# Optimization experiments

Hardware: AMD Instinct MI355X
Metric: run time of the kernel (lower is better)

## Reference

```python
import jax, jax.numpy as jnp
import numpy as np

B = 16; IMG = 127; INC = 64; GROUP = 1; STRIDE = 2; PAD = 1; KS = 3
G = INC // GROUP            # number of ScannCore blocks
S = KS * KS                 # patch_size (attention dim) = 9
SPN = (IMG + 2 * PAD - KS) // STRIDE + 1   # 64
PN = SPN * SPN              # patch_num = 4096
L = GROUP * PN              # sequence length per core


def setup_inputs() -> dict:
    key = jax.random.key(0)
    ks = jax.random.split(key, 9)
    sc = 1.0 / np.sqrt(S)
    x = jax.random.normal(ks[0], (B, INC, IMG, IMG), jnp.float32)
    Wq = jax.random.uniform(ks[1], (G, S, S), jnp.float32, -sc, sc)
    bq = jax.random.uniform(ks[2], (G, S), jnp.float32, -sc, sc)
    Wk = jax.random.uniform(ks[3], (G, S, S), jnp.float32, -sc, sc)
    bk = jax.random.uniform(ks[4], (G, S), jnp.float32, -sc, sc)
    Wv = jax.random.uniform(ks[5], (G, S, S), jnp.float32, -sc, sc)
    bv = jax.random.uniform(ks[6], (G, S), jnp.float32, -sc, sc)
    Wo = jax.random.uniform(ks[7], (G, S, 1), jnp.float32, -sc, sc)
    bo = jax.random.uniform(ks[8], (G, 1), jnp.float32, -sc, sc)
    return dict(x=x, Wq=Wq, bq=bq, Wk=Wk, bk=bk, Wv=Wv, bv=bv, Wo=Wo, bo=bo)


def reference(x, Wq, bq, Wk, bk, Wv, bv, Wo, bo):
    # F.unfold equivalent: [B, INC*S, SPN, SPN] with feature dim ordered (C, kh, kw)
    patches = jax.lax.conv_general_dilated_patches(
        x, (KS, KS), (STRIDE, STRIDE), [(PAD, PAD), (PAD, PAD)])
    t = patches.reshape(B, INC, S, PN)
    # split channels into G groups of GROUP, move patch axis before patch-pixel axis
    t = t.reshape(B, G, GROUP, S, PN).transpose(0, 1, 2, 4, 3).reshape(B, G, L, S)
    # batched tiny single-head attention across all G cores at once
    Q = jnp.einsum('bgls,gst->bglt', t, Wq) + bq[None, :, None, :]
    Km = jnp.einsum('bgls,gst->bglt', t, Wk) + bk[None, :, None, :]
    V = jnp.einsum('bgls,gst->bglt', t, Wv) + bv[None, :, None, :]
    # energy = K^T @ Q over the L axis -> [B, G, S, S]
    energy = jnp.einsum('bgls,bglt->bgst', Km, Q)
    attn = jax.nn.softmax(energy, axis=-1)   # dropout is identity in eval
    # (attn @ V^T)^T -> [B, G, L, S]
    a = jnp.einsum('bgst,bglt->bgls', attn, V)
    out = jnp.einsum('bgls,gso->bglo', a, Wo) + bo[None, :, None, :]  # [B,G,L,1]
    # faithful reshape/permute of original: [B, spn, spn, group] -> [B, group, spn, spn]
    out = out.reshape(B, G, SPN, SPN, GROUP).transpose(0, 1, 4, 2, 3)
    return out.reshape(B, INC, SPN, SPN)
```

## Files before the change

kernel.cpp:

```cpp
#include <hip/hip_runtime.h>
#include <math.h>

#define NB       16
#define IMG      127
#define PLANE    (IMG * IMG)
#define INC      64
#define PN       4096
#define NTHREADS 512
#define PPT      8

#define GLOBAL_AS __attribute__((address_space(1)))
#define LDS_AS    __attribute__((address_space(3)))

__device__ __forceinline__ constexpr int symidx(int p, int q) {
    return p * 9 - (p * (p - 1)) / 2 + (q - p);
}

__device__ __forceinline__ float wave_reduce_sum(float v) {
#define DPP_ADD(ctrl)                                                          \
    v += __builtin_bit_cast(float, __builtin_amdgcn_update_dpp(                \
             0, __builtin_bit_cast(int, v), (ctrl), 0xf, 0xf, true))
    DPP_ADD(0x111);
    DPP_ADD(0x112);
    DPP_ADD(0x114);
    DPP_ADD(0x118);
    DPP_ADD(0x142);
    DPP_ADD(0x143);
#undef DPP_ADD
    return v;
}

#define LOAD_ROW(d0, d1, d2, ihv)                                              \
    {                                                                          \
        const int  ih_ = (ihv);                                                \
        const bool rok = (unsigned)ih_ < (unsigned)IMG;                        \
        const int  ba  = ih_ * IMG + iw0;                                      \
        d0 = (rok && c0) ? plane[ba]     : 0.f;                                \
        d1 =  rok        ? plane[ba + 1] : 0.f;                                \
        d2 = (rok && c2) ? plane[ba + 2] : 0.f;                                \
    }

__global__ void __launch_bounds__(NTHREADS, 4)
scann_fused(const float* __restrict__ x,
            const float* __restrict__ Wq, const float* __restrict__ bq,
            const float* __restrict__ Wk, const float* __restrict__ bk,
            const float* __restrict__ Wv, const float* __restrict__ bv,
            const float* __restrict__ Wo, const float* __restrict__ bo,
            float* __restrict__ out)
{
    __shared__ float plane[PLANE];
    __shared__ float red[8 * 54];
    __shared__ float Msh[45];
    __shared__ float msh[9];
    __shared__ float MW[81];
    __shared__ float Wq_s[81], Wk_s[81], Wv_s[81];
    __shared__ float bq_s[9], bk_s[9], bv_s[9], Wo_s[9];
    __shared__ float en[81], at[81], wt[9], u_s[9];
    __shared__ float c_s, bo_sh;

    const int bg  = blockIdx.x;
    const int g   = bg & 63;
    const int tid = threadIdx.x;
    const int ow  = tid & 63;
    const int wv  = tid >> 6;
    const int oh0 = wv * PPT;

    const float* __restrict__ xp = x + (size_t)bg * PLANE;

    const int a0 = (4 - (bg & 3)) & 3;
    if (tid < a0) plane[tid] = xp[tid];
    #pragma unroll
    for (int j = 0; j < 7; ++j) {
        __builtin_amdgcn_global_load_lds(
            (const GLOBAL_AS void*)(xp + a0 + (j * NTHREADS + tid) * 4),
            (LDS_AS void*)(&plane[a0 + (j * NTHREADS + wv * 64) * 4]), 16, 0, 0);
    }
    {
        const int base = a0 + 7 * NTHREADS * 4;
        const int cnt  = PLANE - base;
        for (int i = tid; i < cnt; i += NTHREADS)
            plane[base + i] = xp[base + i];
    }

    if (tid < 81) {
        Wq_s[tid] = Wq[g * 81 + tid];
        Wk_s[tid] = Wk[g * 81 + tid];
        Wv_s[tid] = Wv[g * 81 + tid];
    } else if (tid >= 128 && tid < 137) {
        const int i = tid - 128;
        bq_s[i] = bq[g * 9 + i];
        bk_s[i] = bk[g * 9 + i];
        bv_s[i] = bv[g * 9 + i];
        Wo_s[i] = Wo[g * 9 + i];
    } else if (tid == 192) {
        bo_sh = bo[g];
    }
    __syncthreads();

    const int  iw0 = ow * 2 - 1;
    const bool c0  = (ow > 0), c2 = (ow < 63);
    const int  ih0 = oh0 * 2 - 1;

    {
        float mA[24], mm[9], v[9];
        #pragma unroll
        for (int i = 0; i < 24; ++i) mA[i] = 0.f;
        #pragma unroll
        for (int i = 0; i < 9; ++i)  mm[i] = 0.f;
        LOAD_ROW(v[0], v[1], v[2], ih0 + 0);
        LOAD_ROW(v[3], v[4], v[5], ih0 + 1);
        LOAD_ROW(v[6], v[7], v[8], ih0 + 2);
        #pragma unroll
        for (int k = 0; k < PPT; ++k) {
            #pragma unroll
            for (int p = 0; p < 9; ++p) mm[p] += v[p];
            int idx = 0;
            #pragma unroll
            for (int p = 0; p < 3; ++p)
                #pragma unroll
                for (int q = p; q < 9; ++q)
                    mA[idx++] += v[p] * v[q];
            if (k < PPT - 1) {
                v[0] = v[6]; v[1] = v[7]; v[2] = v[8];
                LOAD_ROW(v[3], v[4], v[5], ih0 + 2 * (k + 1) + 1);
                LOAD_ROW(v[6], v[7], v[8], ih0 + 2 * (k + 1) + 2);
            }
        }
        #pragma unroll
        for (int i = 0; i < 24; ++i) mA[i] = wave_reduce_sum(mA[i]);
        #pragma unroll
        for (int i = 0; i < 9; ++i)  mm[i] = wave_reduce_sum(mm[i]);
        if (ow == 63) {
            #pragma unroll
            for (int i = 0; i < 24; ++i) red[wv * 54 + i]      = mA[i];
            #pragma unroll
            for (int i = 0; i < 9; ++i)  red[wv * 54 + 45 + i] = mm[i];
        }
    }

    {
        float mB[21], v[9];
        #pragma unroll
        for (int i = 0; i < 21; ++i) mB[i] = 0.f;
        LOAD_ROW(v[0], v[1], v[2], ih0 + 0);
        LOAD_ROW(v[3], v[4], v[5], ih0 + 1);
        LOAD_ROW(v[6], v[7], v[8], ih0 + 2);
        #pragma unroll
        for (int k = 0; k < PPT; ++k) {
            int idx = 0;
            #pragma unroll
            for (int p = 3; p < 9; ++p)
                #pragma unroll
                for (int q = p; q < 9; ++q)
                    mB[idx++] += v[p] * v[q];
            if (k < PPT - 1) {
                v[0] = v[6]; v[1] = v[7]; v[2] = v[8];
                LOAD_ROW(v[3], v[4], v[5], ih0 + 2 * (k + 1) + 1);
                LOAD_ROW(v[6], v[7], v[8], ih0 + 2 * (k + 1) + 2);
            }
        }
        #pragma unroll
        for (int i = 0; i < 21; ++i) mB[i] = wave_reduce_sum(mB[i]);
        if (ow == 63) {
            #pragma unroll
            for (int i = 0; i < 21; ++i) red[wv * 54 + 24 + i] = mB[i];
        }
    }
    __syncthreads();

    if (wv == 0) {
        const int lane = ow;
        if (lane < 54) {
            float s = 0.f;
            #pragma unroll
            for (int w = 0; w < 8; ++w) s += red[w * 54 + lane];
            if (lane < 45) Msh[lane]      = s;
            else           msh[lane - 45] = s;
        }
        #pragma unroll
        for (int r = 0; r < 2; ++r) {
            const int e = lane + r * 64;
            if (e < 81) {
                const int p = e / 9, t = e % 9;
                float acc = 0.f;
                #pragma unroll
                for (int q = 0; q < 9; ++q) {
                    const int a_ = p < q ? p : q, b_ = p < q ? q : p;
                    acc += Msh[symidx(a_, b_)] * Wq_s[q * 9 + t];
                }
                MW[e] = acc;
            }
        }
        #pragma unroll
        for (int r = 0; r < 2; ++r) {
            const int e = lane + r * 64;
            if (e < 81) {
                const int s = e / 9, t = e % 9;
                float km = 0.f, qm = 0.f, acc = 0.f;
                #pragma unroll
                for (int p = 0; p < 9; ++p) {
                    km  += Wk_s[p * 9 + s] * msh[p];
                    qm  += Wq_s[p * 9 + t] * msh[p];
                    acc += Wk_s[p * 9 + s] * MW[p * 9 + t];
                }
                en[e] = acc + (float)PN * bk_s[s] * bq_s[t] + km * bq_s[t] + bk_s[s] * qm;
            }
        }
        if (lane < 9) {
            const int s = lane;
            float mx = en[s * 9];
            #pragma unroll
            for (int t = 1; t < 9; ++t) mx = fmaxf(mx, en[s * 9 + t]);
            float ex[9], sum = 0.f;
            #pragma unroll
            for (int t = 0; t < 9; ++t) { ex[t] = expf(en[s * 9 + t] - mx); sum += ex[t]; }
            const float inv = 1.f / sum;
            #pragma unroll
            for (int t = 0; t < 9; ++t) at[s * 9 + t] = ex[t] * inv;
        }
        if (lane < 9) {
            const int t = lane;
            float w = 0.f;
            #pragma unroll
            for (int s = 0; s < 9; ++s) w += at[s * 9 + t] * Wo_s[s];
            wt[t] = w;
        }
        if (lane < 9) {
            const int p = lane;
            float uu = 0.f;
            #pragma unroll
            for (int t = 0; t < 9; ++t) uu += Wv_s[p * 9 + t] * wt[t];
            u_s[p] = uu;
        }
        if (lane == 12) {
            float cc = bo_sh;
            #pragma unroll
            for (int t = 0; t < 9; ++t) cc += bv_s[t] * wt[t];
            c_s = cc;
        }
    }
    __syncthreads();

    float ur[9];
    #pragma unroll
    for (int i = 0; i < 9; ++i) ur[i] = u_s[i];
    const float cc = c_s;
    float* __restrict__ op = out + (size_t)bg * PN;

    {
        float v[9];
        LOAD_ROW(v[0], v[1], v[2], ih0 + 0);
        LOAD_ROW(v[3], v[4], v[5], ih0 + 1);
        LOAD_ROW(v[6], v[7], v[8], ih0 + 2);
        #pragma unroll
        for (int k = 0; k < PPT; ++k) {
            float o = cc;
            #pragma unroll
            for (int i = 0; i < 9; ++i) o += v[i] * ur[i];
            op[(oh0 + k) * 64 + ow] = o;
            if (k < PPT - 1) {
                v[0] = v[6]; v[1] = v[7]; v[2] = v[8];
                LOAD_ROW(v[3], v[4], v[5], ih0 + 2 * (k + 1) + 1);
                LOAD_ROW(v[6], v[7], v[8], ih0 + 2 * (k + 1) + 2);
            }
        }
    }
}

extern "C" void kernel_launch(void* const* d_in, const int* in_sizes, int n_in,
                              void* d_out, int out_size, void* d_ws, size_t ws_size,
                              hipStream_t stream) {
    (void)in_sizes; (void)n_in; (void)d_ws; (void)ws_size; (void)out_size;
    const float* x  = (const float*)d_in[0];
    const float* Wq = (const float*)d_in[1];
    const float* bq = (const float*)d_in[2];
    const float* Wk = (const float*)d_in[3];
    const float* bk = (const float*)d_in[4];
    const float* Wv = (const float*)d_in[5];
    const float* bv = (const float*)d_in[6];
    const float* Wo = (const float*)d_in[7];
    const float* bo = (const float*)d_in[8];
    float* out = (float*)d_out;

    dim3 grid(NB * INC), block(NTHREADS);
    hipLaunchKernelGGL(scann_fused, grid, block, 0, stream,
                       x, Wq, bq, Wk, bk, Wv, bv, Wo, bo, out);
}
```

Measured before the change: 41.09 us.

## Replace LDS plane staging with bounds-checked raw buffer loads from global

Drops the per-block copy of the whole input plane into shared memory. Each thread now reads its 3x3 patch rows straight from global memory through raw buffer loads, using the buffer's range check to return zero for out-of-bounds padding. Freeing that shared memory allows higher occupancy (launch bounds raised to 8) and cuts the wave reduction to 16-lane partial sums, with 32 slots combined through shared memory. The cost is that the input is read from global/L2 three times (two statistics passes and the output pass) rather than once, and each read depends on cache hit rates.

```diff
diff --git a/kernel.cpp b/kernel.cpp
--- a/kernel.cpp
+++ b/kernel.cpp
@@ -4,19 +4,23 @@
 #define NB       16
 #define IMG      127
 #define PLANE    (IMG * IMG)
+#define ROWB     (IMG * 4)
 #define INC      64
 #define PN       4096
 #define NTHREADS 512
 #define PPT      8
 
-#define GLOBAL_AS __attribute__((address_space(1)))
-#define LDS_AS    __attribute__((address_space(3)))
+typedef int int32x4 __attribute__((ext_vector_type(4)));
+
+__device__ float
+llvm_raw_buffer_load_f32(int32x4 srsrc, int voffset, int soffset, int aux)
+    __asm("llvm.amdgcn.raw.buffer.load.f32");
 
 __device__ __forceinline__ constexpr int symidx(int p, int q) {
     return p * 9 - (p * (p - 1)) / 2 + (q - p);
 }
 
-__device__ __forceinline__ float wave_reduce_sum(float v) {
+__device__ __forceinline__ float wave_reduce16(float v) {
 #define DPP_ADD(ctrl)                                                          \
     v += __builtin_bit_cast(float, __builtin_amdgcn_update_dpp(                \
              0, __builtin_bit_cast(int, v), (ctrl), 0xf, 0xf, true))
@@ -24,23 +28,22 @@
     DPP_ADD(0x112);
     DPP_ADD(0x114);
     DPP_ADD(0x118);
-    DPP_ADD(0x142);
-    DPP_ADD(0x143);
 #undef DPP_ADD
     return v;
 }
 
-#define LOAD_ROW(d0, d1, d2, ihv)                                              \
+#define LOAD_ROW_G(d0, d1, d2, vrow)                                           \
     {                                                                          \
-        const int  ih_ = (ihv);                                                \
-        const bool rok = (unsigned)ih_ < (unsigned)IMG;                        \
-        const int  ba  = ih_ * IMG + iw0;                                      \
-        d0 = (rok && c0) ? plane[ba]     : 0.f;                                \
-        d1 =  rok        ? plane[ba + 1] : 0.f;                                \
-        d2 = (rok && c2) ? plane[ba + 2] : 0.f;                                \
-    }
-
-__global__ void __launch_bounds__(NTHREADS, 4)
+        const int vr_ = (vrow);                                                \
+        const int r0_ = vr_ < 0 ? 0 : vr_;                                     \
+        d0 = llvm_raw_buffer_load_f32(srd, r0_,     0, 0);                     \
+        d1 = llvm_raw_buffer_load_f32(srd, vr_ + 4, 0, 0);                     \
+        d2 = llvm_raw_buffer_load_f32(srd, vr_ + 8, 0, 0);                     \
+        d0 = c0 ? d0 : 0.f;                                                    \
+        d2 = c2 ? d2 : 0.f;                                                    \
+    }
+
+__global__ void __launch_bounds__(NTHREADS, 8)
 scann_fused(const float* __restrict__ x,
             const float* __restrict__ Wq, const float* __restrict__ bq,
             const float* __restrict__ Wk, const float* __restrict__ bk,
@@ -48,8 +51,7 @@
             const float* __restrict__ Wo, const float* __restrict__ bo,
             float* __restrict__ out)
 {
-    __shared__ float plane[PLANE];
-    __shared__ float red[8 * 54];
+    __shared__ float red[32 * 54];
     __shared__ float Msh[45];
     __shared__ float msh[9];
     __shared__ float MW[81];
@@ -66,21 +68,8 @@
     const int oh0 = wv * PPT;
 
     const float* __restrict__ xp = x + (size_t)bg * PLANE;
-
-    const int a0 = (4 - (bg & 3)) & 3;
-    if (tid < a0) plane[tid] = xp[tid];
-    #pragma unroll
-    for (int j = 0; j < 7; ++j) {
-        __builtin_amdgcn_global_load_lds(
-            (const GLOBAL_AS void*)(xp + a0 + (j * NTHREADS + tid) * 4),
-            (LDS_AS void*)(&plane[a0 + (j * NTHREADS + wv * 64) * 4]), 16, 0, 0);
-    }
-    {
-        const int base = a0 + 7 * NTHREADS * 4;
-        const int cnt  = PLANE - base;
-        for (int i = tid; i < cnt; i += NTHREADS)
-            plane[base + i] = xp[base + i];
-    }
+    union { const float* p; unsigned int w[2]; } ba; ba.p = xp;
+    const int32x4 srd = { (int)ba.w[0], (int)ba.w[1], PLANE * 4, 0x00020000 };
 
     if (tid < 81) {
         Wq_s[tid] = Wq[g * 81 + tid];
@@ -95,11 +84,10 @@
     } else if (tid == 192) {
         bo_sh = bo[g];
     }
-    __syncthreads();
-
-    const int  iw0 = ow * 2 - 1;
-    const bool c0  = (ow > 0), c2 = (ow < 63);
-    const int  ih0 = oh0 * 2 - 1;
+
+    const bool c0     = (ow > 0), c2 = (ow < 63);
+    const bool negrow = (oh0 == 0);
+    const int  vb0    = (oh0 * 2 - 1) * ROWB + (ow * 2 - 1) * 4;
 
     {
         float mA[24], mm[9], v[9];
@@ -107,9 +95,10 @@
         for (int i = 0; i < 24; ++i) mA[i] = 0.f;
         #pragma unroll
         for (int i = 0; i < 9; ++i)  mm[i] = 0.f;
-        LOAD_ROW(v[0], v[1], v[2], ih0 + 0);
-        LOAD_ROW(v[3], v[4], v[5], ih0 + 1);
-        LOAD_ROW(v[6], v[7], v[8], ih0 + 2);
+        LOAD_ROW_G(v[0], v[1], v[2], vb0);
+        if (negrow) { v[0] = 0.f; v[1] = 0.f; v[2] = 0.f; }
+        LOAD_ROW_G(v[3], v[4], v[5], vb0 + ROWB);
+        LOAD_ROW_G(v[6], v[7], v[8], vb0 + 2 * ROWB);
         #pragma unroll
         for (int k = 0; k < PPT; ++k) {
             #pragma unroll
@@ -122,19 +111,20 @@
                     mA[idx++] += v[p] * v[q];
             if (k < PPT - 1) {
                 v[0] = v[6]; v[1] = v[7]; v[2] = v[8];
-                LOAD_ROW(v[3], v[4], v[5], ih0 + 2 * (k + 1) + 1);
-                LOAD_ROW(v[6], v[7], v[8], ih0 + 2 * (k + 1) + 2);
-            }
-        }
-        #pragma unroll
-        for (int i = 0; i < 24; ++i) mA[i] = wave_reduce_sum(mA[i]);
-        #pragma unroll
-        for (int i = 0; i < 9; ++i)  mm[i] = wave_reduce_sum(mm[i]);
-        if (ow == 63) {
-            #pragma unroll
-            for (int i = 0; i < 24; ++i) red[wv * 54 + i]      = mA[i];
-            #pragma unroll
-            for (int i = 0; i < 9; ++i)  red[wv * 54 + 45 + i] = mm[i];
+                LOAD_ROW_G(v[3], v[4], v[5], vb0 + (2 * k + 3) * ROWB);
+                LOAD_ROW_G(v[6], v[7], v[8], vb0 + (2 * k + 4) * ROWB);
+            }
+        }
+        #pragma unroll
+        for (int i = 0; i < 24; ++i) mA[i] = wave_reduce16(mA[i]);
+        #pragma unroll
+        for (int i = 0; i < 9; ++i)  mm[i] = wave_reduce16(mm[i]);
+        if ((tid & 15) == 15) {
+            const int slot = tid >> 4;
+            #pragma unroll
+            for (int i = 0; i < 24; ++i) red[slot * 54 + i]      = mA[i];
+            #pragma unroll
+            for (int i = 0; i < 9; ++i)  red[slot * 54 + 45 + i] = mm[i];
         }
     }
 
@@ -142,9 +132,10 @@
         float mB[21], v[9];
         #pragma unroll
         for (int i = 0; i < 21; ++i) mB[i] = 0.f;
-        LOAD_ROW(v[0], v[1], v[2], ih0 + 0);
-        LOAD_ROW(v[3], v[4], v[5], ih0 + 1);
-        LOAD_ROW(v[6], v[7], v[8], ih0 + 2);
+        LOAD_ROW_G(v[0], v[1], v[2], vb0);
+        if (negrow) { v[0] = 0.f; v[1] = 0.f; v[2] = 0.f; }
+        LOAD_ROW_G(v[3], v[4], v[5], vb0 + ROWB);
+        LOAD_ROW_G(v[6], v[7], v[8], vb0 + 2 * ROWB);
         #pragma unroll
         for (int k = 0; k < PPT; ++k) {
             int idx = 0;
@@ -155,15 +146,16 @@
                     mB[idx++] += v[p] * v[q];
             if (k < PPT - 1) {
                 v[0] = v[6]; v[1] = v[7]; v[2] = v[8];
-                LOAD_ROW(v[3], v[4], v[5], ih0 + 2 * (k + 1) + 1);
-                LOAD_ROW(v[6], v[7], v[8], ih0 + 2 * (k + 1) + 2);
-            }
-        }
-        #pragma unroll
-        for (int i = 0; i < 21; ++i) mB[i] = wave_reduce_sum(mB[i]);
-        if (ow == 63) {
-            #pragma unroll
-            for (int i = 0; i < 21; ++i) red[wv * 54 + 24 + i] = mB[i];
+                LOAD_ROW_G(v[3], v[4], v[5], vb0 + (2 * k + 3) * ROWB);
+                LOAD_ROW_G(v[6], v[7], v[8], vb0 + (2 * k + 4) * ROWB);
+            }
+        }
+        #pragma unroll
+        for (int i = 0; i < 21; ++i) mB[i] = wave_reduce16(mB[i]);
+        if ((tid & 15) == 15) {
+            const int slot = tid >> 4;
+            #pragma unroll
+            for (int i = 0; i < 21; ++i) red[slot * 54 + 24 + i] = mB[i];
         }
     }
     __syncthreads();
@@ -173,7 +165,7 @@
         if (lane < 54) {
             float s = 0.f;
             #pragma unroll
-            for (int w = 0; w < 8; ++w) s += red[w * 54 + lane];
+            for (int w = 0; w < 32; ++w) s += red[w * 54 + lane];
             if (lane < 45) Msh[lane]      = s;
             else           msh[lane - 45] = s;
         }
@@ -249,9 +241,10 @@
 
     {
         float v[9];
-        LOAD_ROW(v[0], v[1], v[2], ih0 + 0);
-        LOAD_ROW(v[3], v[4], v[5], ih0 + 1);
-        LOAD_ROW(v[6], v[7], v[8], ih0 + 2);
+        LOAD_ROW_G(v[0], v[1], v[2], vb0);
+        if (negrow) { v[0] = 0.f; v[1] = 0.f; v[2] = 0.f; }
+        LOAD_ROW_G(v[3], v[4], v[5], vb0 + ROWB);
+        LOAD_ROW_G(v[6], v[7], v[8], vb0 + 2 * ROWB);
         #pragma unroll
         for (int k = 0; k < PPT; ++k) {
             float o = cc;
@@ -260,8 +253,8 @@
             op[(oh0 + k) * 64 + ow] = o;
             if (k < PPT - 1) {
                 v[0] = v[6]; v[1] = v[7]; v[2] = v[8];
-                LOAD_ROW(v[3], v[4], v[5], ih0 + 2 * (k + 1) + 1);
-                LOAD_ROW(v[6], v[7], v[8], ih0 + 2 * (k + 1) + 2);
+                LOAD_ROW_G(v[3], v[4], v[5], vb0 + (2 * k + 3) * ROWB);
+                LOAD_ROW_G(v[6], v[7], v[8], vb0 + (2 * k + 4) * ROWB);
             }
         }
     }
```

Measured after the change: 119.9 us. 2.92x slower.
